# Kernel tuning notes

Measured on AMD Instinct MI355X. Metric: run time of the kernel, lower is better.

## Reference

```python
import jax, jax.numpy as jnp
import numpy as np

# Module hyperparameters (init_kwargs)
D = 2          # input_dim
OUT = 3        # output_dim
T = 14         # log2 hash table size
L = 16         # number of levels
F = 2          # features per level
N_MIN, N_MAX = 16, 512
B = 1048576    # batch of query points
HIDDEN = 64

_b = np.exp((np.log(N_MAX) - np.log(N_MIN)) / (L - 1))
RES = jnp.asarray(np.floor(N_MIN * _b ** np.arange(L)).astype(np.float32))  # [L]

# voxel corner offsets [D, 2^D] (same construction as torch module)
_border = np.empty((D, 2 ** D), dtype=np.int32)
for _i in range(D):
    _border[_i, :] = np.array(([0] * 2 ** _i + [1] * 2 ** _i) * 2 ** (D - _i - 1), dtype=np.int32)
BORDER = jnp.asarray(_border)

# NVIDIA tiny-cuda-nn primes; uint32 arithmetic is exact for the low T bits
# (low 14 bits of a product/xor only depend on low 32 bits), matching torch's
# int64 multiply-xor followed by mod 2^T.
PRIMES = jnp.array([1, 2654435761, 805459861, 3674653429, 2097192037, 1434869437, 2165219737][:D], dtype=jnp.uint32)


def setup_inputs() -> dict:
    key = jax.random.key(0)
    ks = jax.random.split(key, 8)
    x = jax.random.uniform(ks[0], (B, D), jnp.float32)  # coords in [0,1)
    tables = jax.random.uniform(ks[1], (L, 2 ** T, F), jnp.float32, -1e-4, 1e-4)
    W1 = jax.random.normal(ks[2], (HIDDEN, L * F), jnp.float32) * 0.05
    b1 = jnp.zeros((HIDDEN,), jnp.float32)
    W2 = jax.random.normal(ks[3], (HIDDEN, HIDDEN), jnp.float32) * 0.05
    b2 = jnp.zeros((HIDDEN,), jnp.float32)
    W3 = jax.random.normal(ks[4], (OUT, HIDDEN), jnp.float32) * 0.05
    b3 = jnp.zeros((OUT,), jnp.float32)
    return {"x": x, "tables": tables, "W1": W1, "b1": b1, "W2": W2, "b2": b2, "W3": W3, "b3": b3}


def reference(x, tables, W1, b1, W2, b2, W3, b3):
    n = x.shape[0]
    # scale coords by each level resolution: [B, D, L]
    scaled = x[:, :, None] * RES[None, None, :]
    grid = jnp.floor(scaled).astype(jnp.int32)                     # [B, D, L]
    corners = grid[..., None] + BORDER[None, :, None, :]           # [B, D, L, 2^D]
    # spatial hash: xor of coord * prime per dimension, mod 2^T
    h = jnp.zeros((n, L, 2 ** D), jnp.uint32)
    for i in range(D):
        h = h ^ (corners[:, i].astype(jnp.uint32) * PRIMES[i])
    idx = (h & jnp.uint32(2 ** T - 1)).astype(jnp.int32)           # [B, L, 2^D]
    # per-level embedding gather: [B, L, 2^D, F]
    looked = tables[jnp.arange(L)[None, :, None], idx]
    # (bi/tri)linear interpolation weights: prod over dims -> [B, L, 2^D]
    w = jnp.prod(1.0 - jnp.abs(scaled[..., None] - corners.astype(x.dtype)), axis=1)
    feat = jnp.einsum('blc,blcf->blf', w, looked).reshape(n, L * F)  # [B, L*F]
    # small MLP head
    h1 = jax.nn.relu(feat @ W1.T + b1)
    h2 = jax.nn.relu(h1 @ W2.T + b2)
    return h2 @ W3.T + b3
```

## Files before the change

### kernel.cpp

```cpp
#include <hip/hip_runtime.h>
#include <hip/hip_bf16.h>
#include <math.h>


#define TBL_MASK 16383u
#define PRIME1   2654435761u

typedef __attribute__((ext_vector_type(8))) short short8;
typedef __attribute__((ext_vector_type(4))) float f32x4;
typedef __attribute__((ext_vector_type(4))) unsigned int uint4v;

struct ResArr { float r[16]; };

__device__ __forceinline__ unsigned short bf16rn(float f) {
    __hip_bfloat16 h = __float2bfloat16(f);
    return __builtin_bit_cast(unsigned short, h);
}
__device__ __forceinline__ float bf16tof(unsigned short u) {
    unsigned int xx = ((unsigned int)u) << 16;
    return __builtin_bit_cast(float, xx);
}
__device__ __forceinline__ short8 ld8(const unsigned short* p) {
    return __builtin_bit_cast(short8, *(const uint4v*)p);
}

#define MFMA(a, b, c) __builtin_amdgcn_mfma_f32_16x16x32_bf16((a), (b), (c), 0, 0, 0)

#define W1H_OFF 0
#define W1L_OFF 2048
#define W2H_OFF 4096
#define W2L_OFF 8192
#define W3H_OFF 12288
#define W3L_OFF 13312
#define WS_USHORTS 14336

__global__ __launch_bounds__(256) void split_weights(
    const float* __restrict__ W1, const float* __restrict__ W2,
    const float* __restrict__ W3, unsigned short* __restrict__ ws)
{
    const int t = blockIdx.x * blockDim.x + threadIdx.x;
    const int stride = gridDim.x * blockDim.x;
    for (int i = t; i < 2048; i += stride) {
        const float v = W1[i];
        const unsigned short hb = bf16rn(v);
        ws[W1H_OFF + i] = hb;
        ws[W1L_OFF + i] = bf16rn(v - bf16tof(hb));
    }
    for (int i = t; i < 4096; i += stride) {
        const float v = W2[i];
        const unsigned short hb = bf16rn(v);
        ws[W2H_OFF + i] = hb;
        ws[W2L_OFF + i] = bf16rn(v - bf16tof(hb));
    }
    for (int i = t; i < 1024; i += stride) {
        const float v = (i < 192) ? W3[i] : 0.0f;
        const unsigned short hb = bf16rn(v);
        ws[W3H_OFF + i] = hb;
        ws[W3L_OFF + i] = bf16rn(v - bf16tof(hb));
    }
}

__global__ __launch_bounds__(64) void mh_mfma(
    const float* __restrict__ x,
    const float* __restrict__ tables,
    const unsigned short* __restrict__ wsw,
    const float* __restrict__ b1,
    const float* __restrict__ b2,
    const float* __restrict__ b3,
    float* __restrict__ out,
    ResArr res, int n)
{
    __shared__ __align__(16) unsigned short smem[7168];
    unsigned short* const sAH = smem;
    unsigned short* const sAL = smem + 2304;

    const int L  = threadIdx.x;
    const int ln = L & 15;
    const int q  = L >> 4;
    const long base = (long)blockIdx.x * 64;
    long s = base + L;
    if (s >= (long)n) s = (long)n - 1;

    const float2 xv = reinterpret_cast<const float2*>(x)[s];
    const float2* __restrict__ tbl2 = reinterpret_cast<const float2*>(tables);

    const int fhb = (L >> 5) * 3328 + L * 40;

    #pragma unroll 4
    for (int l = 0; l < 16; ++l) {
        const float r  = res.r[l];
        const float sx = xv.x * r;
        const float sy = xv.y * r;
        const float gx = floorf(sx);
        const float gy = floorf(sy);
        const unsigned ux = (unsigned)(int)gx;
        const unsigned uy = (unsigned)(int)gy;
        const unsigned hy0 = uy * PRIME1;
        const unsigned hy1 = hy0 + PRIME1;
        const unsigned i00 = ( ux       ^ hy0) & TBL_MASK;
        const unsigned i10 = ((ux + 1u) ^ hy0) & TBL_MASK;
        const unsigned i01 = ( ux       ^ hy1) & TBL_MASK;
        const unsigned i11 = ((ux + 1u) ^ hy1) & TBL_MASK;
        const float2* tl = tbl2 + (l << 14);
        const float2 t00 = tl[i00];
        const float2 t10 = tl[i10];
        const float2 t01 = tl[i01];
        const float2 t11 = tl[i11];
        const float wx0 = 1.0f - fabsf(sx - gx);
        const float wx1 = 1.0f - fabsf(sx - (gx + 1.0f));
        const float wy0 = 1.0f - fabsf(sy - gy);
        const float wy1 = 1.0f - fabsf(sy - (gy + 1.0f));
        const float w00 = wx0 * wy0;
        const float w10 = wx1 * wy0;
        const float w01 = wx0 * wy1;
        const float w11 = wx1 * wy1;
        const float f0 = fmaf(w00, t00.x, fmaf(w10, t10.x, fmaf(w01, t01.x, w11 * t11.x)));
        const float f1 = fmaf(w00, t00.y, fmaf(w10, t10.y, fmaf(w01, t01.y, w11 * t11.y)));
        const unsigned short h0 = bf16rn(f0);
        const unsigned short h1e = bf16rn(f1);
        const unsigned short l0 = bf16rn(f0 - bf16tof(h0));
        const unsigned short l1 = bf16rn(f1 - bf16tof(h1e));
        *(unsigned int*)&smem[fhb + 2 * l]        = (unsigned)h0 | ((unsigned)h1e << 16);
        *(unsigned int*)&smem[fhb + 1280 + 2 * l] = (unsigned)l0 | ((unsigned)l1 << 16);
    }

    float b1v[4], b2v[4];
    #pragma unroll
    for (int nt = 0; nt < 4; ++nt) { b1v[nt] = b1[nt * 16 + ln]; b2v[nt] = b2[nt * 16 + ln]; }
    const float b3v = (ln < 3) ? b3[ln] : 0.0f;

    const f32x4 zero4 = {0.0f, 0.0f, 0.0f, 0.0f};

    for (int mh = 0; mh < 2; ++mh) {
        const int fb = mh ? 4608 : 0;
        short8 a1h[2], a1l[2];
        #pragma unroll
        for (int mt = 0; mt < 2; ++mt) {
            const int row = mt * 16 + ln;
            a1h[mt] = ld8(&smem[fb + row * 40 + q * 8]);
            a1l[mt] = ld8(&smem[fb + 1280 + row * 40 + q * 8]);
        }

        f32x4 acc1[2][4];
        #pragma unroll
        for (int mt = 0; mt < 2; ++mt)
            #pragma unroll
            for (int nt = 0; nt < 4; ++nt) acc1[mt][nt] = zero4;

        #pragma unroll
        for (int nt = 0; nt < 4; ++nt) {
            const short8 bh = ld8(&wsw[W1H_OFF + (nt * 16 + ln) * 32 + q * 8]);
            const short8 bl = ld8(&wsw[W1L_OFF + (nt * 16 + ln) * 32 + q * 8]);
            #pragma unroll
            for (int mt = 0; mt < 2; ++mt) {
                f32x4 a = acc1[mt][nt];
                a = MFMA(a1l[mt], bh, a);
                a = MFMA(a1h[mt], bl, a);
                a = MFMA(a1h[mt], bh, a);
                acc1[mt][nt] = a;
            }
        }
        #pragma unroll
        for (int mt = 0; mt < 2; ++mt)
            #pragma unroll
            for (int nt = 0; nt < 4; ++nt) {
                const int col = nt * 16 + ln;
                #pragma unroll
                for (int r = 0; r < 4; ++r) {
                    float v = fmaxf(acc1[mt][nt][r] + b1v[nt], 0.0f);
                    const unsigned short hb = bf16rn(v);
                    const unsigned short lb = bf16rn(v - bf16tof(hb));
                    const int rl = mt * 16 + q * 4 + r;
                    sAH[rl * 72 + col] = hb;
                    sAL[rl * 72 + col] = lb;
                }
            }

        short8 a2h[2][2], a2l[2][2];
        #pragma unroll
        for (int mt = 0; mt < 2; ++mt)
            #pragma unroll
            for (int ks = 0; ks < 2; ++ks) {
                const int row = mt * 16 + ln;
                a2h[mt][ks] = ld8(&sAH[row * 72 + ks * 32 + q * 8]);
                a2l[mt][ks] = ld8(&sAL[row * 72 + ks * 32 + q * 8]);
            }
        f32x4 acc2[2][4];
        #pragma unroll
        for (int mt = 0; mt < 2; ++mt)
            #pragma unroll
            for (int nt = 0; nt < 4; ++nt) acc2[mt][nt] = zero4;

        #pragma unroll
        for (int nt = 0; nt < 4; ++nt)
            #pragma unroll
            for (int ks = 0; ks < 2; ++ks) {
                const short8 bh = ld8(&wsw[W2H_OFF + (nt * 16 + ln) * 64 + ks * 32 + q * 8]);
                const short8 bl = ld8(&wsw[W2L_OFF + (nt * 16 + ln) * 64 + ks * 32 + q * 8]);
                #pragma unroll
                for (int mt = 0; mt < 2; ++mt) {
                    f32x4 a = acc2[mt][nt];
                    a = MFMA(a2l[mt][ks], bh, a);
                    a = MFMA(a2h[mt][ks], bl, a);
                    a = MFMA(a2h[mt][ks], bh, a);
                    acc2[mt][nt] = a;
                }
            }
        #pragma unroll
        for (int mt = 0; mt < 2; ++mt)
            #pragma unroll
            for (int nt = 0; nt < 4; ++nt) {
                const int col = nt * 16 + ln;
                #pragma unroll
                for (int r = 0; r < 4; ++r) {
                    float v = fmaxf(acc2[mt][nt][r] + b2v[nt], 0.0f);
                    const unsigned short hb = bf16rn(v);
                    const unsigned short lb = bf16rn(v - bf16tof(hb));
                    const int rl = mt * 16 + q * 4 + r;
                    sAH[rl * 72 + col] = hb;
                    sAL[rl * 72 + col] = lb;
                }
            }

        short8 a3h[2][2], a3l[2][2];
        #pragma unroll
        for (int mt = 0; mt < 2; ++mt)
            #pragma unroll
            for (int ks = 0; ks < 2; ++ks) {
                const int row = mt * 16 + ln;
                a3h[mt][ks] = ld8(&sAH[row * 72 + ks * 32 + q * 8]);
                a3l[mt][ks] = ld8(&sAL[row * 72 + ks * 32 + q * 8]);
            }
        f32x4 acc3[2] = {zero4, zero4};
        #pragma unroll
        for (int ks = 0; ks < 2; ++ks) {
            const short8 bh = ld8(&wsw[W3H_OFF + ln * 64 + ks * 32 + q * 8]);
            const short8 bl = ld8(&wsw[W3L_OFF + ln * 64 + ks * 32 + q * 8]);
            #pragma unroll
            for (int mt = 0; mt < 2; ++mt) {
                f32x4 a = acc3[mt];
                a = MFMA(a3l[mt][ks], bh, a);
                a = MFMA(a3h[mt][ks], bl, a);
                a = MFMA(a3h[mt][ks], bh, a);
                acc3[mt] = a;
            }
        }
        if (ln < 3) {
            #pragma unroll
            for (int mt = 0; mt < 2; ++mt)
                #pragma unroll
                for (int r = 0; r < 4; ++r) {
                    const long sg = base + mh * 32 + mt * 16 + q * 4 + r;
                    if (sg < (long)n) out[sg * 3 + ln] = acc3[mt][r] + b3v;
                }
        }
    }
}

extern "C" void kernel_launch(void* const* d_in, const int* in_sizes, int n_in,
                              void* d_out, int out_size, void* d_ws, size_t ws_size,
                              hipStream_t stream) {
    const float* x      = (const float*)d_in[0];
    const float* tables = (const float*)d_in[1];
    const float* W1     = (const float*)d_in[2];
    const float* b1v    = (const float*)d_in[3];
    const float* W2     = (const float*)d_in[4];
    const float* b2v    = (const float*)d_in[5];
    const float* W3     = (const float*)d_in[6];
    const float* b3v    = (const float*)d_in[7];
    float* out = (float*)d_out;
    unsigned short* wsu = (unsigned short*)d_ws;

    const int n = in_sizes[0] / 2;

    ResArr ra;
    const double bb = exp((log(512.0) - log(16.0)) / 15.0);
    for (int k = 0; k < 16; ++k) ra.r[k] = (float)floor(16.0 * pow(bb, (double)k));

    hipLaunchKernelGGL(split_weights, dim3(8), dim3(256), 0, stream, W1, W2, W3, wsu);

    dim3 grid((n + 63) / 64), block(64);
    hipLaunchKernelGGL(mh_mfma, grid, block, 0, stream,
                       x, tables, wsu, b1v, b2v, b3v, out, ra, n);
}
```

Baseline: 259.3 us.

## Compute hash-grid features directly in MFMA A-operand registers, skipping LDS staging

Encoding is now done per MFMA tile instead of per thread over all 16 levels. Each lane computes the 4 levels that its quad position covers, for the rows it owns in the MFMA fragment, and packs the bf16 hi/lo results straight into the A-operand registers. This removes the shared-memory write and read round trip for features and shrinks LDS use. In exchange each lane loads x twice per half-block, and the gather pattern changes, since lanes in different quads now hit different level tables at the same time.

Result: slower. 271.1 us (+4.6%).

```diff
diff --git a/kernel.cpp b/kernel.cpp
--- a/kernel.cpp
+++ b/kernel.cpp
@@ -70,58 +70,25 @@
     float* __restrict__ out,
     ResArr res, int n)
 {
-    __shared__ __align__(16) unsigned short smem[7168];
-    unsigned short* const sAH = smem;
-    unsigned short* const sAL = smem + 2304;
+    __shared__ __align__(16) unsigned short sAH[32 * 72];
+    __shared__ __align__(16) unsigned short sAL[32 * 72];
 
     const int L  = threadIdx.x;
     const int ln = L & 15;
     const int q  = L >> 4;
     const long base = (long)blockIdx.x * 64;
-    long s = base + L;
-    if (s >= (long)n) s = (long)n - 1;
-
-    const float2 xv = reinterpret_cast<const float2*>(x)[s];
+
+    const float2* __restrict__ x2   = reinterpret_cast<const float2*>(x);
     const float2* __restrict__ tbl2 = reinterpret_cast<const float2*>(tables);
 
-    const int fhb = (L >> 5) * 3328 + L * 40;
-
-    #pragma unroll 4
-    for (int l = 0; l < 16; ++l) {
-        const float r  = res.r[l];
-        const float sx = xv.x * r;
-        const float sy = xv.y * r;
-        const float gx = floorf(sx);
-        const float gy = floorf(sy);
-        const unsigned ux = (unsigned)(int)gx;
-        const unsigned uy = (unsigned)(int)gy;
-        const unsigned hy0 = uy * PRIME1;
-        const unsigned hy1 = hy0 + PRIME1;
-        const unsigned i00 = ( ux       ^ hy0) & TBL_MASK;
-        const unsigned i10 = ((ux + 1u) ^ hy0) & TBL_MASK;
-        const unsigned i01 = ( ux       ^ hy1) & TBL_MASK;
-        const unsigned i11 = ((ux + 1u) ^ hy1) & TBL_MASK;
-        const float2* tl = tbl2 + (l << 14);
-        const float2 t00 = tl[i00];
-        const float2 t10 = tl[i10];
-        const float2 t01 = tl[i01];
-        const float2 t11 = tl[i11];
-        const float wx0 = 1.0f - fabsf(sx - gx);
-        const float wx1 = 1.0f - fabsf(sx - (gx + 1.0f));
-        const float wy0 = 1.0f - fabsf(sy - gy);
-        const float wy1 = 1.0f - fabsf(sy - (gy + 1.0f));
-        const float w00 = wx0 * wy0;
-        const float w10 = wx1 * wy0;
-        const float w01 = wx0 * wy1;
-        const float w11 = wx1 * wy1;
-        const float f0 = fmaf(w00, t00.x, fmaf(w10, t10.x, fmaf(w01, t01.x, w11 * t11.x)));
-        const float f1 = fmaf(w00, t00.y, fmaf(w10, t10.y, fmaf(w01, t01.y, w11 * t11.y)));
-        const unsigned short h0 = bf16rn(f0);
-        const unsigned short h1e = bf16rn(f1);
-        const unsigned short l0 = bf16rn(f0 - bf16tof(h0));
-        const unsigned short l1 = bf16rn(f1 - bf16tof(h1e));
-        *(unsigned int*)&smem[fhb + 2 * l]        = (unsigned)h0 | ((unsigned)h1e << 16);
-        *(unsigned int*)&smem[fhb + 1280 + 2 * l] = (unsigned)l0 | ((unsigned)l1 << 16);
+    float rr[4];
+    #pragma unroll
+    for (int t = 0; t < 4; ++t) {
+        const float v0 = res.r[t], v1 = res.r[t + 4];
+        const float v2 = res.r[t + 8], v3 = res.r[t + 12];
+        const float a = (q & 1) ? v1 : v0;
+        const float b = (q & 1) ? v3 : v2;
+        rr[t] = (q & 2) ? b : a;
     }
 
     float b1v[4], b2v[4];
@@ -132,13 +99,54 @@
     const f32x4 zero4 = {0.0f, 0.0f, 0.0f, 0.0f};
 
     for (int mh = 0; mh < 2; ++mh) {
-        const int fb = mh ? 4608 : 0;
         short8 a1h[2], a1l[2];
         #pragma unroll
         for (int mt = 0; mt < 2; ++mt) {
-            const int row = mt * 16 + ln;
-            a1h[mt] = ld8(&smem[fb + row * 40 + q * 8]);
-            a1l[mt] = ld8(&smem[fb + 1280 + row * 40 + q * 8]);
+            long srow = base + mh * 32 + mt * 16 + ln;
+            if (srow >= (long)n) srow = (long)n - 1;
+            const float2 xv = x2[srow];
+            unsigned int hw[4], lw[4];
+            #pragma unroll
+            for (int t = 0; t < 4; ++t) {
+                const float r  = rr[t];
+                const float sx = xv.x * r;
+                const float sy = xv.y * r;
+                const float gx = floorf(sx);
+                const float gy = floorf(sy);
+                const unsigned ux = (unsigned)(int)gx;
+                const unsigned uy = (unsigned)(int)gy;
+                const unsigned hy0 = uy * PRIME1;
+                const unsigned hy1 = hy0 + PRIME1;
+                const unsigned i00 = ( ux       ^ hy0) & TBL_MASK;
+                const unsigned i10 = ((ux + 1u) ^ hy0) & TBL_MASK;
+                const unsigned i01 = ( ux       ^ hy1) & TBL_MASK;
+                const unsigned i11 = ((ux + 1u) ^ hy1) & TBL_MASK;
+                const float2* tl = tbl2 + (((q << 2) + t) << 14);
+                const float2 t00 = tl[i00];
+                const float2 t10 = tl[i10];
+                const float2 t01 = tl[i01];
+                const float2 t11 = tl[i11];
+                const float wx0 = 1.0f - fabsf(sx - gx);
+                const float wx1 = 1.0f - fabsf(sx - (gx + 1.0f));
+                const float wy0 = 1.0f - fabsf(sy - gy);
+                const float wy1 = 1.0f - fabsf(sy - (gy + 1.0f));
+                const float w00 = wx0 * wy0;
+                const float w10 = wx1 * wy0;
+                const float w01 = wx0 * wy1;
+                const float w11 = wx1 * wy1;
+                const float f0 = fmaf(w00, t00.x, fmaf(w10, t10.x, fmaf(w01, t01.x, w11 * t11.x)));
+                const float f1 = fmaf(w00, t00.y, fmaf(w10, t10.y, fmaf(w01, t01.y, w11 * t11.y)));
+                const unsigned short h0 = bf16rn(f0);
+                const unsigned short h1e = bf16rn(f1);
+                const unsigned short l0 = bf16rn(f0 - bf16tof(h0));
+                const unsigned short l1 = bf16rn(f1 - bf16tof(h1e));
+                hw[t] = (unsigned)h0 | ((unsigned)h1e << 16);
+                lw[t] = (unsigned)l0 | ((unsigned)l1 << 16);
+            }
+            const uint4v vh = { hw[0], hw[1], hw[2], hw[3] };
+            const uint4v vl = { lw[0], lw[1], lw[2], lw[3] };
+            a1h[mt] = __builtin_bit_cast(short8, vh);
+            a1l[mt] = __builtin_bit_cast(short8, vl);
         }
 
         f32x4 acc1[2][4];
```
